# Optimization experiments

Hardware: AMD Instinct MI355X
Metric: run time of the kernel (lower is better)

The kernel has to match this reference:

```python
import jax, jax.numpy as jnp
import numpy as np

COMMITMENT_COST = 1.0


def setup_inputs() -> dict:
    key = jax.random.key(0)
    k1, k2 = jax.random.split(key)
    x = jax.random.normal(k1, (8, 4096, 256), dtype=jnp.float32)
    codebook = jax.random.normal(k2, (2048, 256), dtype=jnp.float32)
    return {"x": x, "codebook": codebook}


def reference(x, codebook):
    # Squared Euclidean distances via the GEMM expansion:
    # argmin over torch.cdist (sqrt is monotone); dist values are unused.
    x2 = jnp.sum(x * x, axis=-1, keepdims=True)            # [B, T, 1]
    c2 = jnp.sum(codebook * codebook, axis=-1)             # [N]
    d2 = x2 - 2.0 * jnp.einsum('btd,nd->btn', x, codebook) + c2  # [B, T, N]
    indices = jnp.argmin(d2, axis=-1)                      # [B, T]
    codes = codebook[indices]                              # [B, T, D]

    code_loss = jnp.mean((codes - jax.lax.stop_gradient(x)) ** 2)
    embedding_loss = jnp.mean((x - jax.lax.stop_gradient(codes)) ** 2) * COMMITMENT_COST
    loss = code_loss + embedding_loss

    # Straight-through estimator
    quantized = x + jax.lax.stop_gradient(codes - x)
    return quantized, indices, loss
```

## Files before the change

### kernel.cpp

```cpp
#include <hip/hip_runtime.h>

#define D   256
#define BM  64
#define BN  128
#define KC  64

typedef __attribute__((ext_vector_type(8))) short v8s;
typedef __attribute__((ext_vector_type(4))) float v4f;
#define MFMA16 __builtin_amdgcn_mfma_f32_16x16x32_bf16

static __device__ inline unsigned short f2bf(float f) {
    unsigned u = __float_as_uint(f);
    return (unsigned short)((u + 0x7fffu + ((u >> 16) & 1u)) >> 16);
}
static __device__ inline float bf2f(unsigned short s) {
    return __uint_as_float(((unsigned)s) << 16);
}

static __device__ inline void gl_lds16(const unsigned short* g, unsigned short* l) {
    __builtin_amdgcn_global_load_lds(
        (const __attribute__((address_space(1))) unsigned int*)g,
        (__attribute__((address_space(3))) unsigned int*)l, 16, 0, 0);
}

__global__ void vq_prep_c2(const float* __restrict__ cb, float* __restrict__ c2) {
    const int row  = blockIdx.x;
    const int lane = threadIdx.x;
    const float4 v = *reinterpret_cast<const float4*>(cb + (size_t)row * D + lane * 4);
    float s = v.x * v.x + v.y * v.y + v.z * v.z + v.w * v.w;
    #pragma unroll
    for (int off = 32; off > 0; off >>= 1) s += __shfl_down(s, off, 64);
    if (lane == 0) c2[row] = s;
}

__global__ void vq_prep_sw(const float* __restrict__ cb,
                           unsigned short* __restrict__ cbh, unsigned short* __restrict__ cbl) {
    const int chunk = blockIdx.x;
    const int nc = (chunk >> 2) * BN;
    const int kc = (chunk & 3) * KC;
    #pragma unroll
    for (int i = 0; i < 4; ++i) {
        const int p   = i * 256 + threadIdx.x;
        const int seg = p >> 7;
        const int n   = (p & 127) ^ seg;
        const float* src = cb + (size_t)(nc + n) * D + kc + seg * 8;
        const float4 f0 = *reinterpret_cast<const float4*>(src);
        const float4 f1 = *reinterpret_cast<const float4*>(src + 4);
        const float f[8] = {f0.x, f0.y, f0.z, f0.w, f1.x, f1.y, f1.z, f1.w};
        v8s h, l;
        #pragma unroll
        for (int j = 0; j < 8; ++j) {
            unsigned short hb = f2bf(f[j]);
            h[j] = (short)hb;
            l[j] = (short)f2bf(f[j] - bf2f(hb));
        }
        const size_t o = ((size_t)chunk * 1024 + p) * 8;
        *reinterpret_cast<v8s*>(cbh + o) = h;
        *reinterpret_cast<v8s*>(cbl + o) = l;
    }
}

__global__ __launch_bounds__(256, 2) void vq_argmin_mfma(
        const float* __restrict__ x, const float* __restrict__ cb,
        const unsigned short* __restrict__ cbh, const unsigned short* __restrict__ cbl,
        const float* __restrict__ c2, float* __restrict__ idx_out,
        float* __restrict__ qout, float* __restrict__ partial, int N) {
    __shared__ unsigned short lds_h[2][BN * 8 * 8];
    __shared__ unsigned short lds_l[2][BN * 8 * 8];
    __shared__ float red_v[64 * 32];
    __shared__ int   red_i[64 * 32];

    const int tid  = threadIdx.x;
    const int w    = tid >> 6;
    const int lane = tid & 63;
    const int col  = lane & 15;
    const int quad = lane >> 4;
    const int mg   = w >> 1;
    const int ng   = w & 1;
    const int m0   = blockIdx.x * BM;
    const int n_groups = N >> 7;
    const int n_stages = n_groups * 4;

    const unsigned short* gh0 = cbh + ((size_t)(w * 256 + lane)) * 8;
    const unsigned short* gl0 = cbl + ((size_t)(w * 256 + lane)) * 8;

    #pragma unroll
    for (int i = 0; i < 4; ++i) {
        gl_lds16(gh0 + i * 512, &lds_h[0][(w * 256 + i * 64) * 8]);
        gl_lds16(gl0 + i * 512, &lds_l[0][(w * 256 + i * 64) * 8]);
    }

    v8s xh[2][8], xl[2][8];
    #pragma unroll
    for (int mt = 0; mt < 2; ++mt) {
        const float* xr = x + (size_t)(m0 + mg * 32 + mt * 16 + col) * D;
        #pragma unroll
        for (int ks = 0; ks < 8; ++ks) {
            const int kb = ks * 32 + quad * 8;
            const float4 f0 = *reinterpret_cast<const float4*>(xr + kb);
            const float4 f1 = *reinterpret_cast<const float4*>(xr + kb + 4);
            float f[8] = {f0.x, f0.y, f0.z, f0.w, f1.x, f1.y, f1.z, f1.w};
            v8s h, l;
            #pragma unroll
            for (int j = 0; j < 8; ++j) {
                unsigned short hb = f2bf(f[j]);
                h[j] = (short)hb;
                l[j] = (short)f2bf(f[j] - bf2f(hb));
            }
            xh[mt][ks] = h; xl[mt][ks] = l;
        }
    }

    float runmin[2][4];
    int   runidx[2][4];
    #pragma unroll
    for (int mt = 0; mt < 2; ++mt)
        #pragma unroll
        for (int r = 0; r < 4; ++r) { runmin[mt][r] = 3.4e38f; runidx[mt][r] = 0; }

    v4f acc[4][2];
    #pragma unroll
    for (int nt = 0; nt < 4; ++nt)
        #pragma unroll
        for (int mt = 0; mt < 2; ++mt) acc[nt][mt] = 0.0f;

    for (int g = 0; g < n_groups; ++g) {
        #pragma unroll
        for (int cc = 0; cc < 4; ++cc) {
            const int par   = cc & 1;
            const int stage = g * 4 + cc;
            __syncthreads();
            if (stage + 1 < n_stages) {
                const unsigned short* gh = gh0 + (size_t)(stage + 1) * 8192;
                const unsigned short* gl = gl0 + (size_t)(stage + 1) * 8192;
                unsigned short* lh = lds_h[par ^ 1];
                unsigned short* ll = lds_l[par ^ 1];
                #pragma unroll
                for (int i = 0; i < 4; ++i) {
                    gl_lds16(gh + i * 512, lh + (w * 256 + i * 64) * 8);
                    gl_lds16(gl + i * 512, ll + (w * 256 + i * 64) * 8);
                }
            }

            #pragma unroll
            for (int ksk = 0; ksk < 2; ++ksk) {
                const int ks  = cc * 2 + ksk;
                const int seg = ksk * 4 + quad;
                #pragma unroll
                for (int nt = 0; nt < 4; ++nt) {
                    const int p = seg * BN + ((ng * 64 + nt * 16 + col) ^ seg);
                    const v8s ch = *reinterpret_cast<const v8s*>(&lds_h[par][p * 8]);
                    const v8s cl = *reinterpret_cast<const v8s*>(&lds_l[par][p * 8]);
                    #pragma unroll
                    for (int mt = 0; mt < 2; ++mt) {
                        acc[nt][mt] = MFMA16(xh[mt][ks], ch, acc[nt][mt], 0, 0, 0);
                        acc[nt][mt] = MFMA16(xl[mt][ks], ch, acc[nt][mt], 0, 0, 0);
                        acc[nt][mt] = MFMA16(xh[mt][ks], cl, acc[nt][mt], 0, 0, 0);
                    }
                }
            }
        }

        const int nc = g * BN;
        #pragma unroll
        for (int nt = 0; nt < 4; ++nt) {
            const int n   = nc + ng * 64 + nt * 16 + col;
            const float c2n = c2[n];
            #pragma unroll
            for (int mt = 0; mt < 2; ++mt) {
                #pragma unroll
                for (int r = 0; r < 4; ++r) {
                    const float s = c2n - 2.0f * acc[nt][mt][r];
                    if (s < runmin[mt][r]) { runmin[mt][r] = s; runidx[mt][r] = n; }
                }
                acc[nt][mt] = 0.0f;
            }
        }
    }

    __syncthreads();
    #pragma unroll
    for (int mt = 0; mt < 2; ++mt)
        #pragma unroll
        for (int r = 0; r < 4; ++r) {
            const int row  = mg * 32 + mt * 16 + quad * 4 + r;
            const int slot = (ng * 16 + col) ^ (row & 31);
            red_v[row * 32 + slot] = runmin[mt][r];
            red_i[row * 32 + slot] = runidx[mt][r];
        }
    __syncthreads();
    float best = 3.4e38f;
    int   bidx = 0;
    if (tid < 64) {
        #pragma unroll 4
        for (int t = 0; t < 32; ++t) {
            const int  sl = t ^ (tid & 31);
            const float v = red_v[tid * 32 + sl];
            const int  id = red_i[tid * 32 + sl];
            if (v < best || (v == best && id < bidx)) { best = v; bidx = id; }
        }
        idx_out[m0 + tid] = (float)bidx;
    }
    __syncthreads();
    int* idx_sh = reinterpret_cast<int*>(red_v);
    if (tid < 64) idx_sh[tid] = bidx;
    __syncthreads();

    const float* xg2 = x + (size_t)m0 * D;
    float s = 0.0f;
    #pragma unroll
    for (int i = 0; i < 16; ++i) {
        const int g   = i * 256 + tid;
        const int row = g >> 6;
        const int k4  = (g & 63) * 4;
        const int idx = idx_sh[row];
        const float4 c  = *reinterpret_cast<const float4*>(cb  + (size_t)idx * D + k4);
        const float4 xv = *reinterpret_cast<const float4*>(xg2 + (size_t)row * D + k4);
        *reinterpret_cast<float4*>(qout + (size_t)(m0 + row) * D + k4) = c;
        const float dx = c.x - xv.x, dy = c.y - xv.y, dz = c.z - xv.z, dw = c.w - xv.w;
        s += dx * dx + dy * dy + dz * dz + dw * dw;
    }
    #pragma unroll
    for (int off = 32; off > 0; off >>= 1) s += __shfl_down(s, off, 64);
    float* wsum = reinterpret_cast<float*>(red_i);
    if ((tid & 63) == 0) wsum[tid >> 6] = s;
    __syncthreads();
    if (tid == 0) partial[blockIdx.x] = wsum[0] + wsum[1] + wsum[2] + wsum[3];
}

__global__ void vq_reduce_kernel(const float* __restrict__ partial, float* __restrict__ loss,
                                 float scale, int n) {
    __shared__ float red[4];
    const int tid = threadIdx.x;
    float s = 0.0f;
    for (int i = tid; i < n; i += 256) s += partial[i];
    #pragma unroll
    for (int off = 32; off > 0; off >>= 1) s += __shfl_down(s, off, 64);
    if ((tid & 63) == 0) red[tid >> 6] = s;
    __syncthreads();
    if (tid == 0) loss[0] = (red[0] + red[1] + red[2] + red[3]) * scale;
}

extern "C" void kernel_launch(void* const* d_in, const int* in_sizes, int n_in,
                              void* d_out, int out_size, void* d_ws, size_t ws_size,
                              hipStream_t stream) {
    const float* x  = (const float*)d_in[0];
    const float* cb = (const float*)d_in[1];
    const int M = in_sizes[0] / D;
    const int N = in_sizes[1] / D;

    float* qout    = (float*)d_out;
    float* idx_out = qout + (size_t)M * D;
    float* loss    = idx_out + M;

    char* wsb = (char*)d_ws;
    float*          c2      = (float*)wsb;
    unsigned short* cbh     = (unsigned short*)(wsb + 8192);
    unsigned short* cbl     = cbh + (size_t)N * D;
    float*          partial = (float*)(wsb + 8192 + 2 * (size_t)N * D * sizeof(unsigned short));

    vq_prep_c2<<<N, 64, 0, stream>>>(cb, c2);
    vq_prep_sw<<<(N / BN) * (D / KC), 256, 0, stream>>>(cb, cbh, cbl);
    vq_argmin_mfma<<<M / BM, 256, 0, stream>>>(x, cb, cbh, cbl, c2, idx_out, qout, partial, N);
    const float scale = 2.0f / (float)((size_t)M * D);
    vq_reduce_kernel<<<1, 256, 0, stream>>>(partial, loss, scale, M / BM);
}
```

Baseline: 197.3 us.

## Deepen codebook LDS pipeline to four slots and fuse prep and loss kernels

The two codebook prep kernels are merged into one, and the final loss reduction moves into the argmin kernel through an atomic last-block pattern, which removes launches. The main loop switches to smaller stages in a four-slot LDS ring with a prefetch distance of two, waiting on vmcnt plus a raw barrier instead of a full syncthreads. The c2 norms are staged in LDS, and the cross-wave argmin merge now uses lane shuffles instead of a large LDS table. The cost is more LDS per block, which may reduce occupancy, and correctness now depends on the hand-placed waitcnt and barrier ordering.

New measurement: 209.6 us. +6.2%, slower.

```diff
diff --git a/kernel.cpp b/kernel.cpp
--- a/kernel.cpp
+++ b/kernel.cpp
@@ -3,7 +3,6 @@
 #define D   256
 #define BM  64
 #define BN  128
-#define KC  64
 
 typedef __attribute__((ext_vector_type(8))) short v8s;
 typedef __attribute__((ext_vector_type(4))) float v4f;
@@ -23,52 +22,58 @@
         (__attribute__((address_space(3))) unsigned int*)l, 16, 0, 0);
 }
 
-__global__ void vq_prep_c2(const float* __restrict__ cb, float* __restrict__ c2) {
-    const int row  = blockIdx.x;
-    const int lane = threadIdx.x;
-    const float4 v = *reinterpret_cast<const float4*>(cb + (size_t)row * D + lane * 4);
-    float s = v.x * v.x + v.y * v.y + v.z * v.z + v.w * v.w;
-    #pragma unroll
-    for (int off = 32; off > 0; off >>= 1) s += __shfl_down(s, off, 64);
-    if (lane == 0) c2[row] = s;
-}
-
-__global__ void vq_prep_sw(const float* __restrict__ cb,
-                           unsigned short* __restrict__ cbh, unsigned short* __restrict__ cbl) {
-    const int chunk = blockIdx.x;
-    const int nc = (chunk >> 2) * BN;
-    const int kc = (chunk & 3) * KC;
+__global__ void vq_prep(const float* __restrict__ cb, float* __restrict__ c2,
+                        unsigned short* __restrict__ cbh, unsigned short* __restrict__ cbl) {
+    const int t    = threadIdx.x;
+    const int code = blockIdx.x * 32 + (t >> 3);
+    const int g    = code >> 7;
+    const int nloc = code & 127;
+    const int o    = t & 7;
+    float s = 0.0f;
     #pragma unroll
     for (int i = 0; i < 4; ++i) {
-        const int p   = i * 256 + threadIdx.x;
-        const int seg = p >> 7;
-        const int n   = (p & 127) ^ seg;
-        const float* src = cb + (size_t)(nc + n) * D + kc + seg * 8;
+        const int ko = i * 8 + o;
+        const float* src = cb + (size_t)code * D + ko * 8;
         const float4 f0 = *reinterpret_cast<const float4*>(src);
         const float4 f1 = *reinterpret_cast<const float4*>(src + 4);
         const float f[8] = {f0.x, f0.y, f0.z, f0.w, f1.x, f1.y, f1.z, f1.w};
         v8s h, l;
         #pragma unroll
         for (int j = 0; j < 8; ++j) {
+            s += f[j] * f[j];
             unsigned short hb = f2bf(f[j]);
             h[j] = (short)hb;
             l[j] = (short)f2bf(f[j] - bf2f(hb));
         }
-        const size_t o = ((size_t)chunk * 1024 + p) * 8;
-        *reinterpret_cast<v8s*>(cbh + o) = h;
-        *reinterpret_cast<v8s*>(cbl + o) = l;
-    }
-}
+        const int stage = g * 8 + (ko >> 2);
+        const int seg   = ko & 3;
+        const size_t G  = (size_t)stage * 512 + seg * 128 + (nloc ^ seg);
+        *reinterpret_cast<v8s*>(cbh + G * 8) = h;
+        *reinterpret_cast<v8s*>(cbl + G * 8) = l;
+    }
+    s += __shfl_down(s, 4, 64);
+    s += __shfl_down(s, 2, 64);
+    s += __shfl_down(s, 1, 64);
+    if (o == 0) c2[code] = s;
+}
+
+#define SLOT_H(i) ((i) == 0 ? sh0 : (i) == 1 ? sh1 : (i) == 2 ? sh2 : sh3)
+#define SLOT_L(i) ((i) == 0 ? sl0 : (i) == 1 ? sl1 : (i) == 2 ? sl2 : sl3)
 
 __global__ __launch_bounds__(256, 2) void vq_argmin_mfma(
         const float* __restrict__ x, const float* __restrict__ cb,
         const unsigned short* __restrict__ cbh, const unsigned short* __restrict__ cbl,
         const float* __restrict__ c2, float* __restrict__ idx_out,
-        float* __restrict__ qout, float* __restrict__ partial, int N) {
-    __shared__ unsigned short lds_h[2][BN * 8 * 8];
-    __shared__ unsigned short lds_l[2][BN * 8 * 8];
-    __shared__ float red_v[64 * 32];
-    __shared__ int   red_i[64 * 32];
+        float* __restrict__ qout, float* __restrict__ partial,
+        int* __restrict__ counter, float* __restrict__ loss, float scale, int N) {
+    __shared__ unsigned short sh0[4096], sh1[4096], sh2[4096], sh3[4096];
+    __shared__ unsigned short sl0[4096], sl1[4096], sl2[4096], sl3[4096];
+    __shared__ float c2s[2048];
+    __shared__ float mrg_v[BM * 2];
+    __shared__ int   mrg_i[BM * 2];
+    __shared__ int   idx_sh[BM];
+    __shared__ float wsum[4];
+    __shared__ int   amLast;
 
     const int tid  = threadIdx.x;
     const int w    = tid >> 6;
@@ -79,15 +84,25 @@
     const int ng   = w & 1;
     const int m0   = blockIdx.x * BM;
     const int n_groups = N >> 7;
-    const int n_stages = n_groups * 4;
-
-    const unsigned short* gh0 = cbh + ((size_t)(w * 256 + lane)) * 8;
-    const unsigned short* gl0 = cbl + ((size_t)(w * 256 + lane)) * 8;
-
-    #pragma unroll
-    for (int i = 0; i < 4; ++i) {
-        gl_lds16(gh0 + i * 512, &lds_h[0][(w * 256 + i * 64) * 8]);
-        gl_lds16(gl0 + i * 512, &lds_l[0][(w * 256 + i * 64) * 8]);
+    const int smask    = n_groups * 8 - 1;
+
+    const unsigned short* gh0 = cbh + ((size_t)(w * 128 + lane)) * 8;
+    const unsigned short* gl0 = cbl + ((size_t)(w * 128 + lane)) * 8;
+
+    gl_lds16(gh0,            sh0 + (w * 128) * 8);
+    gl_lds16(gh0 + 64 * 8,   sh0 + (w * 128 + 64) * 8);
+    gl_lds16(gl0,            sl0 + (w * 128) * 8);
+    gl_lds16(gl0 + 64 * 8,   sl0 + (w * 128 + 64) * 8);
+    gl_lds16(gh0 + 4096,     sh1 + (w * 128) * 8);
+    gl_lds16(gh0 + 4096 + 512, sh1 + (w * 128 + 64) * 8);
+    gl_lds16(gl0 + 4096,     sl1 + (w * 128) * 8);
+    gl_lds16(gl0 + 4096 + 512, sl1 + (w * 128 + 64) * 8);
+
+    {
+        const float4 a = *reinterpret_cast<const float4*>(c2 + tid * 8);
+        const float4 b = *reinterpret_cast<const float4*>(c2 + tid * 8 + 4);
+        *reinterpret_cast<float4*>(&c2s[tid * 8])     = a;
+        *reinterpret_cast<float4*>(&c2s[tid * 8 + 4]) = b;
     }
 
     v8s xh[2][8], xl[2][8];
@@ -124,48 +139,45 @@
         #pragma unroll
         for (int mt = 0; mt < 2; ++mt) acc[nt][mt] = 0.0f;
 
+    asm volatile("s_waitcnt lgkmcnt(0)" ::: "memory");
+
     for (int g = 0; g < n_groups; ++g) {
         #pragma unroll
-        for (int cc = 0; cc < 4; ++cc) {
-            const int par   = cc & 1;
-            const int stage = g * 4 + cc;
-            __syncthreads();
-            if (stage + 1 < n_stages) {
-                const unsigned short* gh = gh0 + (size_t)(stage + 1) * 8192;
-                const unsigned short* gl = gl0 + (size_t)(stage + 1) * 8192;
-                unsigned short* lh = lds_h[par ^ 1];
-                unsigned short* ll = lds_l[par ^ 1];
+        for (int ss = 0; ss < 8; ++ss) {
+            asm volatile("s_waitcnt vmcnt(4)\n\ts_barrier" ::: "memory");
+
+            {
+                const int pstage = (g * 8 + ss + 2) & smask;
+                const unsigned short* gh = gh0 + (size_t)pstage * 4096;
+                const unsigned short* gl = gl0 + (size_t)pstage * 4096;
+                unsigned short* lh = SLOT_H((ss + 2) & 3);
+                unsigned short* ll = SLOT_L((ss + 2) & 3);
+                gl_lds16(gh,           lh + (w * 128) * 8);
+                gl_lds16(gh + 64 * 8,  lh + (w * 128 + 64) * 8);
+                gl_lds16(gl,           ll + (w * 128) * 8);
+                gl_lds16(gl + 64 * 8,  ll + (w * 128 + 64) * 8);
+            }
+            __builtin_amdgcn_sched_barrier(0);
+
+            const unsigned short* LH = SLOT_H(ss & 3);
+            const unsigned short* LL = SLOT_L(ss & 3);
+            #pragma unroll
+            for (int nt = 0; nt < 4; ++nt) {
+                const int p = quad * 128 + ((ng * 64 + nt * 16 + col) ^ quad);
+                const v8s ch = *reinterpret_cast<const v8s*>(&LH[p * 8]);
+                const v8s cl = *reinterpret_cast<const v8s*>(&LL[p * 8]);
                 #pragma unroll
-                for (int i = 0; i < 4; ++i) {
-                    gl_lds16(gh + i * 512, lh + (w * 256 + i * 64) * 8);
-                    gl_lds16(gl + i * 512, ll + (w * 256 + i * 64) * 8);
+                for (int mt = 0; mt < 2; ++mt) {
+                    acc[nt][mt] = MFMA16(xh[mt][ss], ch, acc[nt][mt], 0, 0, 0);
+                    acc[nt][mt] = MFMA16(xl[mt][ss], ch, acc[nt][mt], 0, 0, 0);
+                    acc[nt][mt] = MFMA16(xh[mt][ss], cl, acc[nt][mt], 0, 0, 0);
                 }
             }
-
-            #pragma unroll
-            for (int ksk = 0; ksk < 2; ++ksk) {
-                const int ks  = cc * 2 + ksk;
-                const int seg = ksk * 4 + quad;
-                #pragma unroll
-                for (int nt = 0; nt < 4; ++nt) {
-                    const int p = seg * BN + ((ng * 64 + nt * 16 + col) ^ seg);
-                    const v8s ch = *reinterpret_cast<const v8s*>(&lds_h[par][p * 8]);
-                    const v8s cl = *reinterpret_cast<const v8s*>(&lds_l[par][p * 8]);
-                    #pragma unroll
-                    for (int mt = 0; mt < 2; ++mt) {
-                        acc[nt][mt] = MFMA16(xh[mt][ks], ch, acc[nt][mt], 0, 0, 0);
-                        acc[nt][mt] = MFMA16(xl[mt][ks], ch, acc[nt][mt], 0, 0, 0);
-                        acc[nt][mt] = MFMA16(xh[mt][ks], cl, acc[nt][mt], 0, 0, 0);
-                    }
-                }
-            }
-        }
-
-        const int nc = g * BN;
+        }
         #pragma unroll
         for (int nt = 0; nt < 4; ++nt) {
-            const int n   = nc + ng * 64 + nt * 16 + col;
-            const float c2n = c2[n];
+            const int n   = g * BN + ng * 64 + nt * 16 + col;
+            const float c2n = c2s[n];
             #pragma unroll
             for (int mt = 0; mt < 2; ++mt) {
                 #pragma unroll
@@ -178,41 +190,43 @@
         }
     }
 
-    __syncthreads();
     #pragma unroll
     for (int mt = 0; mt < 2; ++mt)
         #pragma unroll
         for (int r = 0; r < 4; ++r) {
-            const int row  = mg * 32 + mt * 16 + quad * 4 + r;
-            const int slot = (ng * 16 + col) ^ (row & 31);
-            red_v[row * 32 + slot] = runmin[mt][r];
-            red_i[row * 32 + slot] = runidx[mt][r];
-        }
-    __syncthreads();
-    float best = 3.4e38f;
-    int   bidx = 0;
+            float v = runmin[mt][r];
+            int  id = runidx[mt][r];
+            #pragma unroll
+            for (int m = 8; m >= 1; m >>= 1) {
+                const float ov = __shfl_xor(v, m, 64);
+                const int   oi = __shfl_xor(id, m, 64);
+                if (ov < v || (ov == v && oi < id)) { v = ov; id = oi; }
+            }
+            if (col == 0) {
+                const int row = mg * 32 + mt * 16 + quad * 4 + r;
+                mrg_v[row * 2 + ng] = v;
+                mrg_i[row * 2 + ng] = id;
+            }
+        }
+    __syncthreads();
     if (tid < 64) {
-        #pragma unroll 4
-        for (int t = 0; t < 32; ++t) {
-            const int  sl = t ^ (tid & 31);
-            const float v = red_v[tid * 32 + sl];
-            const int  id = red_i[tid * 32 + sl];
-            if (v < best || (v == best && id < bidx)) { best = v; bidx = id; }
-        }
+        float best = mrg_v[tid * 2];
+        int   bidx = mrg_i[tid * 2];
+        const float v2 = mrg_v[tid * 2 + 1];
+        const int   i2 = mrg_i[tid * 2 + 1];
+        if (v2 < best || (v2 == best && i2 < bidx)) { best = v2; bidx = i2; }
         idx_out[m0 + tid] = (float)bidx;
-    }
-    __syncthreads();
-    int* idx_sh = reinterpret_cast<int*>(red_v);
-    if (tid < 64) idx_sh[tid] = bidx;
+        idx_sh[tid] = bidx;
+    }
     __syncthreads();
 
     const float* xg2 = x + (size_t)m0 * D;
     float s = 0.0f;
     #pragma unroll
     for (int i = 0; i < 16; ++i) {
-        const int g   = i * 256 + tid;
-        const int row = g >> 6;
-        const int k4  = (g & 63) * 4;
+        const int gq  = i * 256 + tid;
+        const int row = gq >> 6;
+        const int k4  = (gq & 63) * 4;
         const int idx = idx_sh[row];
         const float4 c  = *reinterpret_cast<const float4*>(cb  + (size_t)idx * D + k4);
         const float4 xv = *reinterpret_cast<const float4*>(xg2 + (size_t)row * D + k4);
@@ -222,23 +236,24 @@
     }
     #pragma unroll
     for (int off = 32; off > 0; off >>= 1) s += __shfl_down(s, off, 64);
-    float* wsum = reinterpret_cast<float*>(red_i);
     if ((tid & 63) == 0) wsum[tid >> 6] = s;
     __syncthreads();
-    if (tid == 0) partial[blockIdx.x] = wsum[0] + wsum[1] + wsum[2] + wsum[3];
-}
-
-__global__ void vq_reduce_kernel(const float* __restrict__ partial, float* __restrict__ loss,
-                                 float scale, int n) {
-    __shared__ float red[4];
-    const int tid = threadIdx.x;
-    float s = 0.0f;
-    for (int i = tid; i < n; i += 256) s += partial[i];
-    #pragma unroll
-    for (int off = 32; off > 0; off >>= 1) s += __shfl_down(s, off, 64);
-    if ((tid & 63) == 0) red[tid >> 6] = s;
-    __syncthreads();
-    if (tid == 0) loss[0] = (red[0] + red[1] + red[2] + red[3]) * scale;
+    if (tid == 0) {
+        partial[blockIdx.x] = wsum[0] + wsum[1] + wsum[2] + wsum[3];
+        __threadfence();
+        amLast = (atomicAdd(counter, 1) == (int)gridDim.x - 1);
+    }
+    __syncthreads();
+    if (amLast) {
+        __threadfence();
+        float t = 0.0f;
+        for (int i = tid; i < (int)gridDim.x; i += 256) t += partial[i];
+        #pragma unroll
+        for (int off = 32; off > 0; off >>= 1) t += __shfl_down(t, off, 64);
+        if ((tid & 63) == 0) wsum[tid >> 6] = t;
+        __syncthreads();
+        if (tid == 0) loss[0] = (wsum[0] + wsum[1] + wsum[2] + wsum[3]) * scale;
+    }
 }
 
 extern "C" void kernel_launch(void* const* d_in, const int* in_sizes, int n_in,
@@ -258,10 +273,11 @@
     unsigned short* cbh     = (unsigned short*)(wsb + 8192);
     unsigned short* cbl     = cbh + (size_t)N * D;
     float*          partial = (float*)(wsb + 8192 + 2 * (size_t)N * D * sizeof(unsigned short));
-
-    vq_prep_c2<<<N, 64, 0, stream>>>(cb, c2);
-    vq_prep_sw<<<(N / BN) * (D / KC), 256, 0, stream>>>(cb, cbh, cbl);
-    vq_argmin_mfma<<<M / BM, 256, 0, stream>>>(x, cb, cbh, cbl, c2, idx_out, qout, partial, N);
+    int*            counter = (int*)(partial + M / BM);
+
+    hipMemsetAsync(counter, 0, sizeof(int), stream);
+    vq_prep<<<N / 32, 256, 0, stream>>>(cb, c2, cbh, cbl);
     const float scale = 2.0f / (float)((size_t)M * D);
-    vq_reduce_kernel<<<1, 256, 0, stream>>>(partial, loss, scale, M / BM);
-}
+    vq_argmin_mfma<<<M / BM, 256, 0, stream>>>(x, cb, cbh, cbl, c2, idx_out, qout,
+                                               partial, counter, loss, scale, N);
+}
```
